# Kernel tuning notes

Hardware: AMD Instinct MI355X
Metric: run time of the kernel (lower is better)

The kernel has to match this reference:

```python
import jax, jax.numpy as jnp
import numpy as np
import math

B, N, M = 128, 32, 64           # batch, num_agents, num_other
OBS, ACT = 128, 16              # obs_input_dim, num_actions
D_QK = 128                      # obs_output_dim (== obs_output_dim_other)
D_AV = 64                       # obs_act_output_dim (== other)
F_IN = OBS + ACT                # obs_act_input_dim = 144


def _xavier(key, shape):
    fan_in, fan_out = shape[0], shape[1]
    limit = math.sqrt(6.0 / (fan_in + fan_out))
    return jax.random.uniform(key, shape, jnp.float32, -limit, limit)


def setup_inputs() -> dict:
    key = jax.random.key(0)
    ks = jax.random.split(key, 13)
    return {
        "states": jax.random.normal(ks[0], (B, N, OBS), jnp.float32),
        "policies": jax.random.uniform(ks[1], (B, N, ACT), jnp.float32),
        "actions": jax.random.uniform(ks[2], (B, N, ACT), jnp.float32),
        "states_other": jax.random.normal(ks[3], (B, M, OBS), jnp.float32),
        "actions_other": jax.random.uniform(ks[4], (B, M, ACT), jnp.float32),
        # weights stored as [in, out] (x @ W == nn.Linear without bias)
        "W_key": _xavier(ks[5], (OBS, D_QK)),
        "W_query": _xavier(ks[6], (OBS, D_QK)),
        "W_av": _xavier(ks[7], (F_IN, D_AV)),
        "W_key_other": _xavier(ks[8], (OBS, D_QK)),
        "W_query_other": _xavier(ks[9], (OBS, D_QK)),
        "W_av_other": _xavier(ks[10], (F_IN, D_AV)),
        "W_f1": _xavier(ks[11], (2 * D_AV, 64)),
        "W_f2": _xavier(ks[12], (64, 1)),
    }


def reference(states, policies, actions, states_other, actions_other,
              W_key, W_query, W_av, W_key_other, W_query_other,
              W_av_other, W_f1, W_f2):
    b, n, _ = states.shape
    obs_actions = jnp.concatenate([states, actions], axis=-1)   # [B,N,F_IN]
    obs_policy = jnp.concatenate([states, policies], axis=-1)   # [B,N,F_IN]

    key_obs = states @ W_key                                    # [B,N,D_QK]
    query_obs = states @ W_query                                # [B,N,D_QK]
    d_k = W_key.shape[1]
    weight = jax.nn.softmax(
        jnp.einsum('bid,bjd->bij', query_obs, key_obs) / math.sqrt(d_k), axis=-1)
    ret_weight = weight

    # place_policies is identity on (j,k): oap[b,j,k] = obs_policy[b,k] if j==k else obs_actions[b,k]
    eye = jnp.eye(n, dtype=states.dtype)[None, :, :, None]       # [1,N,N,1]
    oap = eye * obs_policy[:, None, :, :] + (1.0 - eye) * obs_actions[:, None, :, :]
    attention_values = jnp.tanh(oap @ W_av)                      # [B,N,N,D_AV] (j,k)

    # repeat-mul-sum == weighted reduction over k: wav[b,i,j,d] = sum_k w[b,i,k] av[b,j,k,d]
    wav = jnp.einsum('bik,bjkd->bijd', weight, attention_values)  # [B,N,N,D_AV]

    obs_actions_other = jnp.concatenate([states_other, actions_other], axis=-1)
    keys_other = states_other @ W_key_other                      # [B,M,D_QK]
    query_agent = states @ W_query_other                         # [B,N,D_QK]
    av_other = jnp.tanh(obs_actions_other @ W_av_other)          # [B,M,D_AV]
    d_k_o = W_key_other.shape[1]
    weight_other = jax.nn.softmax(
        jnp.einsum('bid,bmd->bim', query_agent, keys_other) / math.sqrt(d_k_o), axis=-1)
    wav_other = jnp.einsum('bim,bmd->bid', weight_other, av_other)  # [B,N,D_AV]

    # broadcast the per-agent other-branch features across the j axis for the concat
    wav_other_b = jnp.broadcast_to(wav_other[:, :, None, :], wav.shape[:-1] + (wav_other.shape[-1],))
    node_features = jnp.concatenate([wav, wav_other_b], axis=-1)  # [B,N,N,2*D_AV]

    h = jax.nn.leaky_relu(node_features @ W_f1, negative_slope=0.01)
    value = h @ W_f2                                              # [B,N,N,1]
    return value, ret_weight, weight_other
```

## Files before the change

### kernel.cpp

```cpp
#include <hip/hip_runtime.h>
#include <math.h>

#define WS_WQK   0
#define WS_WQKO  16384
#define WS_AVA   32768
#define WS_AVO   294912
#define WS_DPROJ 819200

#define INV_SQRT_DK 0.08838834764831845f

__device__ __forceinline__ float dot4(float4 a, float4 b) {
  return a.x*b.x + a.y*b.y + a.z*b.z + a.w*b.w;
}
__device__ __forceinline__ void fma4(float4& a, const float4 w, const float s) {
  a.x += w.x*s; a.y += w.y*s; a.z += w.z*s; a.w += w.w*s;
}

__global__ __launch_bounds__(256, 2) void k1_pre(
    const float* __restrict__ g_states, const float* __restrict__ g_pol,
    const float* __restrict__ g_act, const float* __restrict__ g_so,
    const float* __restrict__ g_ao,
    const float* __restrict__ Wq, const float* __restrict__ Wk,
    const float* __restrict__ Wqo, const float* __restrict__ Wko,
    const float* __restrict__ W_av, const float* __restrict__ W_avo,
    const float* __restrict__ W_f1, float* __restrict__ ws)
{
  __shared__ __align__(16) float pool[8448];
  const int t = threadIdx.x;
  int blk = blockIdx.x;

  if (blk < 32) {
    const float* A; const float* Bm; float* O;
    if (blk < 16) { A = Wq;  Bm = Wk;  O = ws + WS_WQK; }
    else          { A = Wqo; Bm = Wko; O = ws + WS_WQKO; blk -= 16; }
    const int tr = (blk >> 2) << 5;
    const int tc = (blk & 3) << 5;
    float* sA = pool;
    float* sB = pool + 4224;
    const float4* a4 = (const float4*)(A + tr * 128);
    const float4* b4 = (const float4*)(Bm + tc * 128);
    #pragma unroll
    for (int u = 0; u < 4; ++u) {
      int f = t + u * 256;
      int r = f >> 5, c4 = f & 31;
      *(float4*)(sA + r*132 + c4*4) = a4[f];
      *(float4*)(sB + r*132 + c4*4) = b4[f];
    }
    __syncthreads();
    const int e = t & 31, cl0 = t >> 5;
    float acc[4] = {0,0,0,0};
    #pragma unroll 4
    for (int d4 = 0; d4 < 32; ++d4) {
      float4 bv = *(const float4*)(sB + e*132 + d4*4);
      #pragma unroll
      for (int rr = 0; rr < 4; ++rr) {
        float4 av = *(const float4*)(sA + (cl0 + rr*8)*132 + d4*4);
        acc[rr] += dot4(av, bv);
      }
    }
    #pragma unroll
    for (int rr = 0; rr < 4; ++rr)
      O[(tr + cl0 + rr*8)*128 + tc + e] = acc[rr];
    return;
  }
  blk -= 32;

  if (blk < 256) {
    const int b  = blk >> 1;
    const int jh = blk & 1;
    float* s_in  = pool;
    float* s_t   = pool + 2112;
    float* s_pre = pool + 2752;
    float* s_dl  = pool + 4864;
    {
      const float4* gs4 = (const float4*)(g_states + b*4096 + jh*2048);
      #pragma unroll
      for (int u = 0; u < 2; ++u) {
        int f = t + u * 256;
        int r = f >> 5, c4 = f & 31;
        *(float4*)(s_in + r*132 + c4*4) = gs4[f];
      }
      if (t < 64) {
        int r = t >> 2, c4 = t & 3;
        *(float4*)(s_t + r*40 + c4*4) =
            ((const float4*)(g_act + b*512 + jh*256))[t];
      } else if (t < 128) {
        int t2 = t - 64;
        int r = t2 >> 2, c4 = t2 & 3;
        *(float4*)(s_t + r*40 + 20 + c4*4) =
            ((const float4*)(g_pol + b*512 + jh*256))[t2];
      }
    }
    __syncthreads();
    {
      const int wv_  = t >> 6;
      const int ap   = wv_ & 1;
      const int rq   = wv_ >> 1;
      const int lane = t & 63;
      const float* s_rows = s_in + rq*8*132;
      const float* s_tl   = s_t + rq*8*40 + ap*20;
      float acc[8];
      #pragma unroll
      for (int r = 0; r < 8; ++r) acc[r] = 0.f;
      #pragma unroll 4
      for (int c4 = 0; c4 < 32; ++c4) {
        const float w0 = W_av[(c4*4+0)*64 + lane];
        const float w1 = W_av[(c4*4+1)*64 + lane];
        const float w2 = W_av[(c4*4+2)*64 + lane];
        const float w3 = W_av[(c4*4+3)*64 + lane];
        #pragma unroll
        for (int r = 0; r < 8; ++r) {
          float4 sv = *(const float4*)(s_rows + r*132 + c4*4);
          acc[r] += sv.x*w0 + sv.y*w1 + sv.z*w2 + sv.w*w3;
        }
      }
      #pragma unroll
      for (int c4 = 0; c4 < 4; ++c4) {
        const float w0 = W_av[(128 + c4*4+0)*64 + lane];
        const float w1 = W_av[(128 + c4*4+1)*64 + lane];
        const float w2 = W_av[(128 + c4*4+2)*64 + lane];
        const float w3 = W_av[(128 + c4*4+3)*64 + lane];
        #pragma unroll
        for (int r = 0; r < 8; ++r) {
          float4 sv = *(const float4*)(s_tl + r*40 + c4*4);
          acc[r] += sv.x*w0 + sv.y*w1 + sv.z*w2 + sv.w*w3;
        }
      }
      #pragma unroll
      for (int r = 0; r < 8; ++r)
        s_pre[(rq*8 + r)*132 + ap*64 + lane] = acc[r];
    }
    __syncthreads();
    {
      const int r = t >> 4, d0 = (t & 15) << 2;
      float4 a0 = *(const float4*)(s_pre + r*132 + d0);
      float4 p0 = *(const float4*)(s_pre + r*132 + 64 + d0);
      float4 va0, dl0;
      va0.x = tanhf(a0.x); va0.y = tanhf(a0.y); va0.z = tanhf(a0.z); va0.w = tanhf(a0.w);
      dl0.x = tanhf(p0.x) - va0.x; dl0.y = tanhf(p0.y) - va0.y;
      dl0.z = tanhf(p0.z) - va0.z; dl0.w = tanhf(p0.w) - va0.w;
      *(float4*)(ws + WS_AVA + b*2048 + (jh*16 + r)*64 + d0) = va0;
      *(float4*)(s_dl + r*68 + d0) = dl0;
    }
    __syncthreads();
    {
      const int h = t & 63;
      const int j0 = (t >> 6) << 2;
      float acc[4] = {0,0,0,0};
      #pragma unroll 4
      for (int d4 = 0; d4 < 16; ++d4) {
        float w0 = W_f1[(d4*4+0)*64 + h];
        float w1 = W_f1[(d4*4+1)*64 + h];
        float w2 = W_f1[(d4*4+2)*64 + h];
        float w3 = W_f1[(d4*4+3)*64 + h];
        #pragma unroll
        for (int q = 0; q < 4; ++q) {
          float4 dv = *(const float4*)(s_dl + (j0+q)*68 + d4*4);
          acc[q] += dv.x*w0 + dv.y*w1 + dv.z*w2 + dv.w*w3;
        }
      }
      #pragma unroll
      for (int q = 0; q < 4; ++q)
        ws[WS_DPROJ + b*2048 + (jh*16 + j0+q)*64 + h] = acc[q];
    }
    return;
  }
  blk -= 256;

  {
    const int b = blk >> 2, m0 = (blk & 3) << 4;
    float* s_so = pool;
    float* s_ao = pool + 2112;
    {
      const float4* gso4 = (const float4*)(g_so + (b*64 + m0) * 128);
      #pragma unroll
      for (int u = 0; u < 2; ++u) {
        int f = t + u * 256;
        int r = f >> 5, c4 = f & 31;
        *(float4*)(s_so + r*132 + c4*4) = gso4[f];
      }
      if (t < 64) {
        int r = t >> 2, c4 = t & 3;
        *(float4*)(s_ao + r*20 + c4*4) =
            ((const float4*)(g_ao + (b*64 + m0)*16))[t];
      }
    }
    __syncthreads();
    const int wv_  = t >> 6;
    const int lane = t & 63;
    const float* s_rows = s_so + wv_*4*132;
    const float* s_tl   = s_ao + wv_*4*20;
    float acc[4] = {0.f, 0.f, 0.f, 0.f};
    #pragma unroll 4
    for (int c4 = 0; c4 < 32; ++c4) {
      const float w0 = W_avo[(c4*4+0)*64 + lane];
      const float w1 = W_avo[(c4*4+1)*64 + lane];
      const float w2 = W_avo[(c4*4+2)*64 + lane];
      const float w3 = W_avo[(c4*4+3)*64 + lane];
      #pragma unroll
      for (int r = 0; r < 4; ++r) {
        float4 sv = *(const float4*)(s_rows + r*132 + c4*4);
        acc[r] += sv.x*w0 + sv.y*w1 + sv.z*w2 + sv.w*w3;
      }
    }
    #pragma unroll
    for (int c4 = 0; c4 < 4; ++c4) {
      const float w0 = W_avo[(128 + c4*4+0)*64 + lane];
      const float w1 = W_avo[(128 + c4*4+1)*64 + lane];
      const float w2 = W_avo[(128 + c4*4+2)*64 + lane];
      const float w3 = W_avo[(128 + c4*4+3)*64 + lane];
      #pragma unroll
      for (int r = 0; r < 4; ++r) {
        float4 sv = *(const float4*)(s_tl + r*20 + c4*4);
        acc[r] += sv.x*w0 + sv.y*w1 + sv.z*w2 + sv.w*w3;
      }
    }
    #pragma unroll
    for (int r = 0; r < 4; ++r)
      ws[WS_AVO + b*4096 + (m0 + wv_*4 + r)*64 + lane] = tanhf(acc[r]);
  }
}

__global__ __launch_bounds__(512, 4) void k2_main(
    const float* __restrict__ g_states, const float* __restrict__ g_so,
    const float* __restrict__ W_f1, const float* __restrict__ W_f2,
    const float* __restrict__ ws, float* __restrict__ out)
{
  __shared__ __align__(16) float pool[17472];
  float* s_st   = pool;
  float* s_red  = pool + 4352;
  float* s_avA  = pool + 4352;
  float* s_dp   = pool + 6528;
  float* s_avO  = pool;
  float* s_P    = pool + 12800;
  float* s_w    = pool + 14944;
  float* s_wo   = pool + 15232;
  float* s_S    = pool + 15776;
  float* s_wavo = pool + 16320;
  float* s_base = pool + 16864;
  float* s_wf2  = pool + 17408;

  const int t = threadIdx.x;
  const int b = blockIdx.x >> 2;
  const int i0 = (blockIdx.x & 3) << 3;

  {
    const float4* gs4 = (const float4*)(g_states + b * 4096);
    #pragma unroll
    for (int u = 0; u < 2; ++u) {
      int f = t + u * 512;
      int r = f >> 5, c4 = f & 31;
      *(float4*)(s_st + r*132 + c4*4) = gs4[f];
    }
    if (t < 16) *(float4*)(s_wf2 + t*4) = ((const float4*)W_f2)[t];
  }
  __syncthreads();

  {
    const int wave = t >> 6;
    const int kc   = wave & 3;
    const int rh   = wave >> 2;
    const int col  = t & 63;
    const float* Wp = (col < 32) ? (ws + WS_WQK + col*4)
                                 : (ws + WS_WQKO + (col-32)*4);
    const float* srow = s_st + (i0 + rh*4)*132 + kc*32;
    float4 acc[4];
    #pragma unroll
    for (int r = 0; r < 4; ++r) acc[r] = make_float4(0.f,0.f,0.f,0.f);
    #pragma unroll 2
    for (int c4 = 0; c4 < 8; ++c4) {
      float4 sv[4];
      #pragma unroll
      for (int r = 0; r < 4; ++r)
        sv[r] = *(const float4*)(srow + r*132 + c4*4);
      #pragma unroll
      for (int k = 0; k < 4; ++k) {
        float4 wv = *(const float4*)(Wp + (kc*32 + c4*4 + k)*128);
        #pragma unroll
        for (int r = 0; r < 4; ++r)
          fma4(acc[r], wv, ((const float*)&sv[r])[k]);
      }
    }
    #pragma unroll
    for (int r = 0; r < 4; ++r)
      *(float4*)(s_red + ((kc*8 + rh*4 + r)*66 + col)*4) = acc[r];
  }
  __syncthreads();
  {
    const int r = t >> 6, col = t & 63;
    float4 a0 = *(const float4*)(s_red + ((0*8 + r)*66 + col)*4);
    float4 a1 = *(const float4*)(s_red + ((1*8 + r)*66 + col)*4);
    float4 a2 = *(const float4*)(s_red + ((2*8 + r)*66 + col)*4);
    float4 a3 = *(const float4*)(s_red + ((3*8 + r)*66 + col)*4);
    float4 s4;
    s4.x = (a0.x + a1.x) + (a2.x + a3.x);
    s4.y = (a0.y + a1.y) + (a2.y + a3.y);
    s4.z = (a0.z + a1.z) + (a2.z + a3.z);
    s4.w = (a0.w + a1.w) + (a2.w + a3.w);
    *(float4*)(s_P + r*268 + col*4) = s4;
  }
  __syncthreads();

  {
    const int r = t >> 6, j = t & 31, half = (t >> 5) & 1;
    const int e0 = half << 4;
    float acc = 0.f;
    #pragma unroll 8
    for (int e4 = 0; e4 < 16; ++e4) {
      float4 p4  = *(const float4*)(s_P + r*268 + (e0 + e4)*4);
      float4 st4 = *(const float4*)(s_st + j*132 + (e0 + e4)*4);
      acc += dot4(p4, st4);
    }
    acc += __shfl_xor(acc, 32, 64);
    acc *= INV_SQRT_DK;
    float mx = acc;
    for (int off = 16; off; off >>= 1) mx = fmaxf(mx, __shfl_xor(mx, off, 32));
    float ev = __expf(acc - mx);
    float sum = ev;
    for (int off = 16; off; off >>= 1) sum += __shfl_xor(sum, off, 32);
    float wn = ev / sum;
    if (half == 0) {
      out[131072 + b*1024 + (i0 + r)*32 + j] = wn;
      s_w[r*36 + j] = wn;
    }
  }
  __syncthreads();

  for (int tt = 0; tt < 2; ++tt) {
    const float4* gt4 = (const float4*)(g_so + (b*64 + tt*32) * 128);
    #pragma unroll
    for (int u = 0; u < 2; ++u) {
      int f = t + u * 512;
      int r = f >> 5, c4 = f & 31;
      *(float4*)(s_st + r*132 + c4*4) = gt4[f];
    }
    __syncthreads();
    const int r = t >> 6, m = t & 31, half = (t >> 5) & 1;
    const int c0 = half << 4;
    float acc = 0.f;
    #pragma unroll 8
    for (int c4 = 0; c4 < 16; ++c4) {
      float4 p4  = *(const float4*)(s_P + r*268 + 128 + (c0 + c4)*4);
      float4 st4 = *(const float4*)(s_st + m*132 + (c0 + c4)*4);
      acc += dot4(p4, st4);
    }
    acc += __shfl_xor(acc, 32, 64);
    if (half == 0) s_wo[r*68 + tt*32 + m] = acc * INV_SQRT_DK;
    __syncthreads();
  }

  {
    const int r = t >> 6, l = t & 63;
    float v = s_wo[r*68 + l];
    float mx = v;
    for (int off = 32; off; off >>= 1) mx = fmaxf(mx, __shfl_xor(mx, off, 64));
    float ev = __expf(v - mx);
    float sum = ev;
    for (int off = 32; off; off >>= 1) sum += __shfl_xor(sum, off, 64);
    float wn = ev / sum;
    out[262144 + b*2048 + (i0 + r)*64 + l] = wn;
    s_wo[r*68 + l] = wn;
  }
  {
    int f = t;
    int k = f >> 4, dq = f & 15;
    *(float4*)(s_avA + k*68 + dq*4) = ((const float4*)(ws + WS_AVA + b*2048))[f];
    *(float4*)(s_dp  + k*68 + dq*4) = ((const float4*)(ws + WS_DPROJ + b*2048))[f];
  }
  #pragma unroll
  for (int u = 0; u < 2; ++u) {
    int f = t + u * 512;
    int m = f >> 4, dq = f & 15;
    *(float4*)(s_avO + m*68 + dq*4) = ((const float4*)(ws + WS_AVO + b*4096))[f];
  }
  __syncthreads();

  if (t < 128) {
    const int i = t >> 4, dq = (t & 15) << 2;
    float4 acc = {0,0,0,0};
    #pragma unroll 4
    for (int k = 0; k < 32; ++k) {
      float4 a4 = *(const float4*)(s_avA + k*68 + dq);
      float wv = s_w[i*36 + k];
      acc.x += wv*a4.x; acc.y += wv*a4.y; acc.z += wv*a4.z; acc.w += wv*a4.w;
    }
    *(float4*)(s_S + i*68 + dq) = acc;
  } else if (t < 384) {
    const int tt2 = t - 128;
    const int mh = tt2 >> 7;
    const int i = (tt2 & 127) >> 4, dq = (tt2 & 15) << 2;
    float4 acc = {0,0,0,0};
    #pragma unroll 4
    for (int mm = 0; mm < 32; ++mm) {
      const int m = mh*32 + mm;
      float4 a4 = *(const float4*)(s_avO + m*68 + dq);
      float wv = s_wo[i*68 + m];
      acc.x += wv*a4.x; acc.y += wv*a4.y; acc.z += wv*a4.z; acc.w += wv*a4.w;
    }
    float* dst = mh ? (s_P + i*68 + dq) : (s_wavo + i*68 + dq);
    *(float4*)dst = acc;
  }
  __syncthreads();

  {
    const int h = t & 63, i = t >> 6;
    float a0 = 0.f;
    #pragma unroll 4
    for (int d = 0; d < 64; ++d) {
      float w1v = W_f1[d*64 + h];
      float w2v = W_f1[(64 + d)*64 + h];
      a0 += s_S[i*68 + d]*w1v + (s_wavo[i*68 + d] + s_P[i*68 + d])*w2v;
    }
    s_base[i*68 + h] = a0;
  }
  __syncthreads();

  {
    const int i = t >> 6, j = t & 31, half = (t >> 5) & 1;
    const float wij = s_w[i*36 + j];
    float acc = 0.f;
    #pragma unroll 4
    for (int hq = half*8; hq < half*8 + 8; ++hq) {
      float4 b4 = *(const float4*)(s_base + i*68 + hq*4);
      float4 d4 = *(const float4*)(s_dp + j*68 + hq*4);
      float4 f4 = *(const float4*)(s_wf2 + hq*4);
      float p0 = b4.x + wij*d4.x; p0 = p0 > 0.f ? p0 : 0.01f*p0;
      float p1 = b4.y + wij*d4.y; p1 = p1 > 0.f ? p1 : 0.01f*p1;
      float p2 = b4.z + wij*d4.z; p2 = p2 > 0.f ? p2 : 0.01f*p2;
      float p3 = b4.w + wij*d4.w; p3 = p3 > 0.f ? p3 : 0.01f*p3;
      acc += p0*f4.x + p1*f4.y + p2*f4.z + p3*f4.w;
    }
    acc += __shfl_xor(acc, 32, 64);
    if (half == 0)
      out[b*1024 + (i0 + i)*32 + j] = acc;
  }
}

extern "C" void kernel_launch(void* const* d_in, const int* in_sizes, int n_in,
                              void* d_out, int out_size, void* d_ws, size_t ws_size,
                              hipStream_t stream) {
  const float* states        = (const float*)d_in[0];
  const float* policies      = (const float*)d_in[1];
  const float* actions       = (const float*)d_in[2];
  const float* states_other  = (const float*)d_in[3];
  const float* actions_other = (const float*)d_in[4];
  const float* W_key         = (const float*)d_in[5];
  const float* W_query       = (const float*)d_in[6];
  const float* W_av          = (const float*)d_in[7];
  const float* W_key_other   = (const float*)d_in[8];
  const float* W_query_other = (const float*)d_in[9];
  const float* W_av_other    = (const float*)d_in[10];
  const float* W_f1          = (const float*)d_in[11];
  const float* W_f2          = (const float*)d_in[12];
  float* out = (float*)d_out;
  float* ws  = (float*)d_ws;

  k1_pre<<<800, 256, 0, stream>>>(states, policies, actions, states_other,
                                  actions_other, W_query, W_key,
                                  W_query_other, W_key_other, W_av, W_av_other,
                                  W_f1, ws);
  k2_main<<<512, 512, 0, stream>>>(states, states_other, W_f1, W_f2, ws, out);
}
```

Measured before the change: 120.1 us.

## Split k1 agent blocks finer, swizzle k2 shared memory, prefetch states_other

The agent-value section of k1 now uses four blocks per batch instead of two, each covering 8 rows. The grid grows from 800 to 1056 blocks to spread the tanh/projection work more widely. In k2, shared-memory tiles for states, states_other and dproj use an XOR column swizzle to reduce bank conflicts. states_other is prefetched into registers during the self-attention softmax and then processed in one 64-wide pass, which removes a loop with two extra barriers. The k2 launch-bounds occupancy hint is lowered from 4 to 2, which gives more registers per thread at the cost of resident waves.

```diff
diff --git a/kernel.cpp b/kernel.cpp
--- a/kernel.cpp
+++ b/kernel.cpp
@@ -8,6 +8,9 @@
 #define WS_DPROJ 819200
 
 #define INV_SQRT_DK 0.08838834764831845f
+
+#define SWZ32(row, c) (((c) ^ ((row) >> 3)) & 31)
+#define SWZ16(row, c) (((c) ^ ((row) >> 3)) & 15)
 
 __device__ __forceinline__ float dot4(float4 a, float4 b) {
   return a.x*b.x + a.y*b.y + a.z*b.z + a.w*b.w;
@@ -65,30 +68,26 @@
   }
   blk -= 32;
 
-  if (blk < 256) {
-    const int b  = blk >> 1;
-    const int jh = blk & 1;
+  if (blk < 512) {
+    const int b  = blk >> 2;
+    const int jq = blk & 3;
     float* s_in  = pool;
-    float* s_t   = pool + 2112;
-    float* s_pre = pool + 2752;
-    float* s_dl  = pool + 4864;
+    float* s_t   = pool + 1056;
+    float* s_pre = pool + 1376;
+    float* s_dl  = pool + 2432;
     {
-      const float4* gs4 = (const float4*)(g_states + b*4096 + jh*2048);
-      #pragma unroll
-      for (int u = 0; u < 2; ++u) {
-        int f = t + u * 256;
-        int r = f >> 5, c4 = f & 31;
-        *(float4*)(s_in + r*132 + c4*4) = gs4[f];
-      }
-      if (t < 64) {
-        int r = t >> 2, c4 = t & 3;
-        *(float4*)(s_t + r*40 + c4*4) =
-            ((const float4*)(g_act + b*512 + jh*256))[t];
-      } else if (t < 128) {
-        int t2 = t - 64;
-        int r = t2 >> 2, c4 = t2 & 3;
-        *(float4*)(s_t + r*40 + 20 + c4*4) =
-            ((const float4*)(g_pol + b*512 + jh*256))[t2];
+      const float4* gs4 = (const float4*)(g_states + b*4096 + jq*1024);
+      int r = t >> 5, c4 = t & 31;
+      *(float4*)(s_in + r*132 + c4*4) = gs4[t];
+      if (t < 32) {
+        int rr = t >> 2, cc = t & 3;
+        *(float4*)(s_t + rr*40 + cc*4) =
+            ((const float4*)(g_act + b*512 + jq*128))[t];
+      } else if (t < 64) {
+        int t2 = t - 32;
+        int rr = t2 >> 2, cc = t2 & 3;
+        *(float4*)(s_t + rr*40 + 20 + cc*4) =
+            ((const float4*)(g_pol + b*512 + jq*128))[t2];
       }
     }
     __syncthreads();
@@ -97,11 +96,9 @@
       const int ap   = wv_ & 1;
       const int rq   = wv_ >> 1;
       const int lane = t & 63;
-      const float* s_rows = s_in + rq*8*132;
-      const float* s_tl   = s_t + rq*8*40 + ap*20;
-      float acc[8];
-      #pragma unroll
-      for (int r = 0; r < 8; ++r) acc[r] = 0.f;
+      const float* s_rows = s_in + rq*4*132;
+      const float* s_tl   = s_t + rq*4*40 + ap*20;
+      float acc[4] = {0,0,0,0};
       #pragma unroll 4
       for (int c4 = 0; c4 < 32; ++c4) {
         const float w0 = W_av[(c4*4+0)*64 + lane];
@@ -109,7 +106,7 @@
         const float w2 = W_av[(c4*4+2)*64 + lane];
         const float w3 = W_av[(c4*4+3)*64 + lane];
         #pragma unroll
-        for (int r = 0; r < 8; ++r) {
+        for (int r = 0; r < 4; ++r) {
           float4 sv = *(const float4*)(s_rows + r*132 + c4*4);
           acc[r] += sv.x*w0 + sv.y*w1 + sv.z*w2 + sv.w*w3;
         }
@@ -121,17 +118,17 @@
         const float w2 = W_av[(128 + c4*4+2)*64 + lane];
         const float w3 = W_av[(128 + c4*4+3)*64 + lane];
         #pragma unroll
-        for (int r = 0; r < 8; ++r) {
+        for (int r = 0; r < 4; ++r) {
           float4 sv = *(const float4*)(s_tl + r*40 + c4*4);
           acc[r] += sv.x*w0 + sv.y*w1 + sv.z*w2 + sv.w*w3;
         }
       }
       #pragma unroll
-      for (int r = 0; r < 8; ++r)
-        s_pre[(rq*8 + r)*132 + ap*64 + lane] = acc[r];
+      for (int r = 0; r < 4; ++r)
+        s_pre[(rq*4 + r)*132 + ap*64 + lane] = acc[r];
     }
     __syncthreads();
-    {
+    if (t < 128) {
       const int r = t >> 4, d0 = (t & 15) << 2;
       float4 a0 = *(const float4*)(s_pre + r*132 + d0);
       float4 p0 = *(const float4*)(s_pre + r*132 + 64 + d0);
@@ -139,14 +136,14 @@
       va0.x = tanhf(a0.x); va0.y = tanhf(a0.y); va0.z = tanhf(a0.z); va0.w = tanhf(a0.w);
       dl0.x = tanhf(p0.x) - va0.x; dl0.y = tanhf(p0.y) - va0.y;
       dl0.z = tanhf(p0.z) - va0.z; dl0.w = tanhf(p0.w) - va0.w;
-      *(float4*)(ws + WS_AVA + b*2048 + (jh*16 + r)*64 + d0) = va0;
+      *(float4*)(ws + WS_AVA + b*2048 + (jq*8 + r)*64 + d0) = va0;
       *(float4*)(s_dl + r*68 + d0) = dl0;
     }
     __syncthreads();
     {
       const int h = t & 63;
-      const int j0 = (t >> 6) << 2;
-      float acc[4] = {0,0,0,0};
+      const int j0 = (t >> 6) << 1;
+      float acc[2] = {0,0};
       #pragma unroll 4
       for (int d4 = 0; d4 < 16; ++d4) {
         float w0 = W_f1[(d4*4+0)*64 + h];
@@ -154,18 +151,18 @@
         float w2 = W_f1[(d4*4+2)*64 + h];
         float w3 = W_f1[(d4*4+3)*64 + h];
         #pragma unroll
-        for (int q = 0; q < 4; ++q) {
+        for (int q = 0; q < 2; ++q) {
           float4 dv = *(const float4*)(s_dl + (j0+q)*68 + d4*4);
           acc[q] += dv.x*w0 + dv.y*w1 + dv.z*w2 + dv.w*w3;
         }
       }
       #pragma unroll
-      for (int q = 0; q < 4; ++q)
-        ws[WS_DPROJ + b*2048 + (jh*16 + j0+q)*64 + h] = acc[q];
+      for (int q = 0; q < 2; ++q)
+        ws[WS_DPROJ + b*2048 + (jq*8 + j0+q)*64 + h] = acc[q];
     }
     return;
   }
-  blk -= 256;
+  blk -= 512;
 
   {
     const int b = blk >> 2, m0 = (blk & 3) << 4;
@@ -221,7 +218,7 @@
   }
 }
 
-__global__ __launch_bounds__(512, 4) void k2_main(
+__global__ __launch_bounds__(512, 2) void k2_main(
     const float* __restrict__ g_states, const float* __restrict__ g_so,
     const float* __restrict__ W_f1, const float* __restrict__ W_f2,
     const float* __restrict__ ws, float* __restrict__ out)
@@ -229,6 +226,7 @@
   __shared__ __align__(16) float pool[17472];
   float* s_st   = pool;
   float* s_red  = pool + 4352;
+  float* s_so   = pool + 4352;
   float* s_avA  = pool + 4352;
   float* s_dp   = pool + 6528;
   float* s_avO  = pool;
@@ -250,7 +248,7 @@
     for (int u = 0; u < 2; ++u) {
       int f = t + u * 512;
       int r = f >> 5, c4 = f & 31;
-      *(float4*)(s_st + r*132 + c4*4) = gs4[f];
+      *(float4*)(s_st + r*132 + 4*SWZ32(r, c4)) = gs4[f];
     }
     if (t < 16) *(float4*)(s_wf2 + t*4) = ((const float4*)W_f2)[t];
   }
@@ -263,16 +261,18 @@
     const int col  = t & 63;
     const float* Wp = (col < 32) ? (ws + WS_WQK + col*4)
                                  : (ws + WS_WQKO + (col-32)*4);
-    const float* srow = s_st + (i0 + rh*4)*132 + kc*32;
+    const int rbase = i0 + rh*4;
+    const int rsw   = i0 >> 3;
     float4 acc[4];
     #pragma unroll
     for (int r = 0; r < 4; ++r) acc[r] = make_float4(0.f,0.f,0.f,0.f);
     #pragma unroll 2
     for (int c4 = 0; c4 < 8; ++c4) {
+      const int colw = 4*(((kc*8 + c4) ^ rsw) & 31);
       float4 sv[4];
       #pragma unroll
       for (int r = 0; r < 4; ++r)
-        sv[r] = *(const float4*)(srow + r*132 + c4*4);
+        sv[r] = *(const float4*)(s_st + (rbase + r)*132 + colw);
       #pragma unroll
       for (int k = 0; k < 4; ++k) {
         float4 wv = *(const float4*)(Wp + (kc*32 + c4*4 + k)*128);
@@ -301,6 +301,12 @@
   }
   __syncthreads();
 
+  float4 stg[4];
+  {
+    const float4* gso4 = (const float4*)(g_so + b * 64 * 128);
+    #pragma unroll
+    for (int u = 0; u < 4; ++u) stg[u] = gso4[t + u*512];
+  }
   {
     const int r = t >> 6, j = t & 31, half = (t >> 5) & 1;
     const int e0 = half << 4;
@@ -308,7 +314,7 @@
     #pragma unroll 8
     for (int e4 = 0; e4 < 16; ++e4) {
       float4 p4  = *(const float4*)(s_P + r*268 + (e0 + e4)*4);
-      float4 st4 = *(const float4*)(s_st + j*132 + (e0 + e4)*4);
+      float4 st4 = *(const float4*)(s_st + j*132 + 4*SWZ32(j, e0 + e4));
       acc += dot4(p4, st4);
     }
     acc += __shfl_xor(acc, 32, 64);
@@ -324,30 +330,28 @@
       s_w[r*36 + j] = wn;
     }
   }
-  __syncthreads();
-
-  for (int tt = 0; tt < 2; ++tt) {
-    const float4* gt4 = (const float4*)(g_so + (b*64 + tt*32) * 128);
-    #pragma unroll
-    for (int u = 0; u < 2; ++u) {
+  {
+    #pragma unroll
+    for (int u = 0; u < 4; ++u) {
       int f = t + u * 512;
-      int r = f >> 5, c4 = f & 31;
-      *(float4*)(s_st + r*132 + c4*4) = gt4[f];
-    }
-    __syncthreads();
-    const int r = t >> 6, m = t & 31, half = (t >> 5) & 1;
-    const int c0 = half << 4;
+      int m = f >> 5, c4 = f & 31;
+      *(float4*)(s_so + m*132 + 4*SWZ32(m, c4)) = stg[u];
+    }
+  }
+  __syncthreads();
+
+  {
+    const int r = t >> 6, m = t & 63;
     float acc = 0.f;
     #pragma unroll 8
-    for (int c4 = 0; c4 < 16; ++c4) {
-      float4 p4  = *(const float4*)(s_P + r*268 + 128 + (c0 + c4)*4);
-      float4 st4 = *(const float4*)(s_st + m*132 + (c0 + c4)*4);
-      acc += dot4(p4, st4);
-    }
-    acc += __shfl_xor(acc, 32, 64);
-    if (half == 0) s_wo[r*68 + tt*32 + m] = acc * INV_SQRT_DK;
-    __syncthreads();
-  }
+    for (int c4 = 0; c4 < 32; ++c4) {
+      float4 p4  = *(const float4*)(s_P + r*268 + 128 + c4*4);
+      float4 so4 = *(const float4*)(s_so + m*132 + 4*SWZ32(m, c4));
+      acc += dot4(p4, so4);
+    }
+    s_wo[r*68 + m] = acc * INV_SQRT_DK;
+  }
+  __syncthreads();
 
   {
     const int r = t >> 6, l = t & 63;
@@ -362,10 +366,10 @@
     s_wo[r*68 + l] = wn;
   }
   {
-    int f = t;
-    int k = f >> 4, dq = f & 15;
-    *(float4*)(s_avA + k*68 + dq*4) = ((const float4*)(ws + WS_AVA + b*2048))[f];
-    *(float4*)(s_dp  + k*68 + dq*4) = ((const float4*)(ws + WS_DPROJ + b*2048))[f];
+    int k = t >> 4, dq = t & 15;
+    *(float4*)(s_avA + k*68 + dq*4) = ((const float4*)(ws + WS_AVA + b*2048))[t];
+    *(float4*)(s_dp  + k*68 + 4*SWZ16(k, dq)) =
+        ((const float4*)(ws + WS_DPROJ + b*2048))[t];
   }
   #pragma unroll
   for (int u = 0; u < 2; ++u) {
@@ -422,7 +426,7 @@
     #pragma unroll 4
     for (int hq = half*8; hq < half*8 + 8; ++hq) {
       float4 b4 = *(const float4*)(s_base + i*68 + hq*4);
-      float4 d4 = *(const float4*)(s_dp + j*68 + hq*4);
+      float4 d4 = *(const float4*)(s_dp + j*68 + 4*SWZ16(j, hq));
       float4 f4 = *(const float4*)(s_wf2 + hq*4);
       float p0 = b4.x + wij*d4.x; p0 = p0 > 0.f ? p0 : 0.01f*p0;
       float p1 = b4.y + wij*d4.y; p1 = p1 > 0.f ? p1 : 0.01f*p1;
@@ -455,9 +459,9 @@
   float* out = (float*)d_out;
   float* ws  = (float*)d_ws;
 
-  k1_pre<<<800, 256, 0, stream>>>(states, policies, actions, states_other,
-                                  actions_other, W_query, W_key,
-                                  W_query_other, W_key_other, W_av, W_av_other,
-                                  W_f1, ws);
+  k1_pre<<<1056, 256, 0, stream>>>(states, policies, actions, states_other,
+                                   actions_other, W_query, W_key,
+                                   W_query_other, W_key_other, W_av, W_av_other,
+                                   W_f1, ws);
   k2_main<<<512, 512, 0, stream>>>(states, states_other, W_f1, W_f2, ws, out);
 }
```

New measurement: 114.5 us. 1.05x faster.
